# Performance work log

Measured on AMD Instinct MI355X. Metric: run time of the kernel, lower is better.

Reference implementation:

```python
import jax, jax.numpy as jnp
import numpy as np

N_NODES = 100000
N_EDGES = 1600000
F_IN = 8
PERIODS = 18
UNITS = 256     # A3TGCN out_channels (unit_num)
HIDDEN = 256    # MLP hidden_units


def setup_inputs() -> dict:
    key = jax.random.key(0)
    ks = jax.random.split(key, 24)
    g = lambda k, shape, s: (jax.random.normal(k, shape, dtype=jnp.float32) * s)
    inp = {
        "x": g(ks[0], (N_NODES, F_IN, PERIODS), 1.0),
        "edge_index": jax.random.randint(ks[1], (2, N_EDGES), 0, N_NODES, dtype=jnp.int64),
        "edge_weight": jax.random.uniform(ks[2], (N_EDGES,), dtype=jnp.float32),
        # TGCN gate params: GCNConv weight/bias + Linear(2*UNITS, UNITS)
        "Wz": g(ks[3], (F_IN, UNITS), 0.1), "bz": jnp.zeros((UNITS,), jnp.float32),
        "Wlz": g(ks[4], (2 * UNITS, UNITS), 0.05), "blz": jnp.zeros((UNITS,), jnp.float32),
        "Wr": g(ks[5], (F_IN, UNITS), 0.1), "br": jnp.zeros((UNITS,), jnp.float32),
        "Wlr": g(ks[6], (2 * UNITS, UNITS), 0.05), "blr": jnp.zeros((UNITS,), jnp.float32),
        "Wh": g(ks[7], (F_IN, UNITS), 0.1), "bh": jnp.zeros((UNITS,), jnp.float32),
        "Wlh": g(ks[8], (2 * UNITS, UNITS), 0.05), "blh": jnp.zeros((UNITS,), jnp.float32),
        # temporal attention logits
        "att": jax.random.uniform(ks[9], (PERIODS,), dtype=jnp.float32),
        # MLP head
        "W1": g(ks[10], (UNITS, HIDDEN), 0.05), "b1": jnp.zeros((HIDDEN,), jnp.float32),
        "W2": g(ks[11], (HIDDEN, HIDDEN), 0.05), "b2": jnp.zeros((HIDDEN,), jnp.float32),
        "W3": g(ks[12], (HIDDEN, HIDDEN), 0.05), "b3": jnp.zeros((HIDDEN,), jnp.float32),
        "Wo": g(ks[13], (HIDDEN, PERIODS), 0.05), "bo": jnp.zeros((PERIODS,), jnp.float32),
    }
    return inp


def _gcn_norm(edge_index, edge_weight, n_nodes):
    # PyG gcn_norm with add_self_loops=True, improved=False
    src, dst = edge_index[0], edge_index[1]
    loop = jnp.arange(n_nodes, dtype=src.dtype)
    src_a = jnp.concatenate([src, loop])
    dst_a = jnp.concatenate([dst, loop])
    w_a = jnp.concatenate([edge_weight, jnp.ones((n_nodes,), edge_weight.dtype)])
    deg = jax.ops.segment_sum(w_a, dst_a, num_segments=n_nodes)
    dinv = jnp.where(deg > 0, jax.lax.rsqrt(jnp.where(deg > 0, deg, 1.0)), 0.0)
    norm = dinv[src_a] * w_a * dinv[dst_a]
    return src_a, dst_a, norm


def reference(x, edge_index, edge_weight, Wz, bz, Wlz, blz, Wr, br, Wlr, blr,
              Wh, bh, Wlh, blh, att, W1, b1, W2, b2, W3, b3, Wo, bo):
    n_nodes = x.shape[0]
    src, dst, norm = _gcn_norm(edge_index, edge_weight, n_nodes)

    def gconv(X, W, b):
        m = (X @ W)[src] * norm[:, None]                       # [E+N, UNITS]
        return jax.ops.segment_sum(m, dst, num_segments=n_nodes) + b

    probs = jax.nn.softmax(att)

    def step(carry, inp):
        H, acc = carry
        Xt, p = inp                                            # Xt: [N, F_IN]
        Z = jax.nn.sigmoid(jnp.concatenate([gconv(Xt, Wz, bz), H], 1) @ Wlz + blz)
        R = jax.nn.sigmoid(jnp.concatenate([gconv(Xt, Wr, br), H], 1) @ Wlr + blr)
        Ht = jnp.tanh(jnp.concatenate([gconv(Xt, Wh, bh), H * R], 1) @ Wlh + blh)
        H = Z * H + (1.0 - Z) * Ht
        return (H, acc + p * H), None

    xs = jnp.transpose(x, (2, 0, 1))                           # [T, N, F_IN]
    init = (jnp.zeros((n_nodes, UNITS), x.dtype), jnp.zeros((n_nodes, UNITS), x.dtype))
    (_, h), _ = jax.lax.scan(step, init, (xs, probs))

    h = jax.nn.relu(h)
    h = jax.nn.relu(h @ W1 + b1)
    h = jax.nn.relu(h @ W2 + b2)
    h = jax.nn.relu(h @ W3 + b3)
    return h @ Wo + bo                                         # [N, PERIODS]
```

## Files before the change

### kernel.cpp

```cpp
#include <hip/hip_runtime.h>

typedef _Float16 h8 __attribute__((ext_vector_type(8)));
typedef _Float16 h2 __attribute__((ext_vector_type(2)));
typedef float f4 __attribute__((ext_vector_type(4)));

#define N_NODES 100000
#define NPAD    100096
#define N_EDGES 1600000
#define T_P  18
#define U    256
#define KP   288
#define LDW  296
#define NB_SCAN 391

#define LOG2E  1.44269504f
#define LOG2E2 2.88539008f

__global__ void k_init_deg(float* deg){
    int i = blockIdx.x*256 + threadIdx.x;
    if (i < N_NODES) deg[i] = 1.0f;
}
__global__ void k_deg(const int* __restrict__ ei, const float* __restrict__ w, float* deg){
    int e = blockIdx.x*256 + threadIdx.x;
    if (e < N_EDGES) atomicAdd(&deg[ei[N_EDGES + e]], w[e]);
}
__global__ void k_dinv(const float* deg, float* dinv){
    int i = blockIdx.x*256 + threadIdx.x;
    if (i < N_NODES) dinv[i] = rsqrtf(deg[i]);
}
__global__ void k_count(const int* __restrict__ ei, int* cnt){
    int e = blockIdx.x*256 + threadIdx.x;
    if (e < N_EDGES) atomicAdd(&cnt[ei[N_EDGES + e]], 1);
}
__global__ void k_partial(const int* __restrict__ cnt, int* part){
    __shared__ int red[256];
    int b = blockIdx.x, i = b*256 + threadIdx.x;
    red[threadIdx.x] = (i < N_NODES) ? cnt[i] : 0;
    __syncthreads();
    for (int d = 128; d > 0; d >>= 1){
        if (threadIdx.x < d) red[threadIdx.x] += red[threadIdx.x + d];
        __syncthreads();
    }
    if (threadIdx.x == 0) part[b] = red[0];
}
__global__ void k_scan_part(const int* __restrict__ part, int* pbase){
    __shared__ int s[512];
    int tid = threadIdx.x;
    int v = (tid < NB_SCAN) ? part[tid] : 0;
    s[tid] = v; __syncthreads();
    for (int d = 1; d < 512; d <<= 1){
        int t2 = (tid >= d) ? s[tid - d] : 0;
        __syncthreads();
        s[tid] += t2;
        __syncthreads();
    }
    if (tid < NB_SCAN) pbase[tid] = s[tid] - v;
}
__global__ void k_emit(const int* __restrict__ cnt, const int* __restrict__ pbase,
                       int* rowp, int* ccur){
    __shared__ int s[256];
    int b = blockIdx.x, tid = threadIdx.x, i = b*256 + tid;
    int v = (i < N_NODES) ? cnt[i] : 0;
    s[tid] = v; __syncthreads();
    for (int d = 1; d < 256; d <<= 1){
        int t2 = (tid >= d) ? s[tid - d] : 0;
        __syncthreads();
        s[tid] += t2;
        __syncthreads();
    }
    int excl = s[tid] - v + pbase[b];
    if (i < N_NODES){
        rowp[i] = excl; ccur[i] = excl;
        if (i == N_NODES - 1) rowp[N_NODES] = excl + v;
    }
}
__global__ void k_scatter(const int* __restrict__ ei, const float* __restrict__ w,
                          const float* __restrict__ dinv, int* ccur,
                          int* __restrict__ csrc, float* __restrict__ cnrm){
    int e = blockIdx.x*256 + threadIdx.x;
    if (e >= N_EDGES) return;
    int s = ei[e], d = ei[N_EDGES + e];
    int pos = atomicAdd(&ccur[d], 1);
    csrc[pos] = s;
    cnrm[pos] = dinv[s] * w[e] * dinv[d];
}
__global__ void k_gather_nf(const float* __restrict__ x, const float* __restrict__ dinv,
                            const int* __restrict__ rowp, const int* __restrict__ csrc,
                            const float* __restrict__ cnrm, _Float16* __restrict__ AXh){
    int idx = blockIdx.x*256 + threadIdx.x;
    if (idx >= N_NODES*8) return;
    int n = idx >> 3, f = idx & 7;
    float dv = dinv[n];
    float w0 = dv * dv;
    const float* xb = x + (size_t)n*144 + f*18;
    float s[T_P];
    #pragma unroll
    for (int t = 0; t < T_P; t++) s[t] = w0 * xb[t];
    int p1 = rowp[n+1];
    for (int p = rowp[n]; p < p1; p++){
        float w = cnrm[p];
        const float* xs = x + (size_t)csrc[p]*144 + f*18;
        #pragma unroll
        for (int t = 0; t < T_P; t++) s[t] += w * xs[t];
    }
    #pragma unroll
    for (int t = 0; t < T_P; t++)
        AXh[((size_t)t*NPAD + n)*8 + f] = (_Float16)s[t];
}

__global__ void k_probs(const float* att, float* probs){
    if (threadIdx.x == 0 && blockIdx.x == 0){
        float mx = -1e30f;
        for (int t = 0; t < T_P; t++) mx = fmaxf(mx, att[t]);
        float e[T_P], s = 0.f;
        for (int t = 0; t < T_P; t++){ e[t] = __expf(att[t] - mx); s += e[t]; }
        for (int t = 0; t < T_P; t++) probs[t] = e[t] / s;
    }
}
__global__ void k_wprime(const float* Wz, const float* bz, const float* Wlz, const float* blz,
                         const float* Wr, const float* br, const float* Wlr, const float* blr,
                         const float* Wh, const float* bh, const float* Wlh, const float* blh,
                         float* wprime, float* biasg){
    int idx = blockIdx.x*256 + threadIdx.x;
    if (idx >= 3*9*256) return;
    int g = idx / (9*256); int rem = idx - g*9*256;
    int row = rem / 256;   int u = rem - row*256;
    const float* W  = g==0 ? Wz  : (g==1 ? Wr  : Wh);
    const float* Wl = g==0 ? Wlz : (g==1 ? Wlr : Wlh);
    const float* bb = g==0 ? bz  : (g==1 ? br  : bh);
    const float* bl = g==0 ? blz : (g==1 ? blr : blh);
    float s = 0.f;
    if (row < 8){
        for (int c = 0; c < U; c++) s += W[row*U + c] * Wl[c*U + u];
        wprime[(g*8 + row)*U + u] = s;
    } else {
        for (int c = 0; c < U; c++) s += bb[c] * Wl[c*U + u];
        biasg[g*U + u] = s + bl[u];
    }
}
__global__ void k_fill_gates(const float* __restrict__ wprime, const float* __restrict__ Wlz,
                             const float* __restrict__ Wlr, const float* __restrict__ Wlh,
                             _Float16* __restrict__ B1t, _Float16* __restrict__ B2t){
    int idx = blockIdx.x*256 + threadIdx.x;
    if (idx >= 768*KP) return;
    int n = idx / KP, k = idx - n*KP;
    int g = (n < 256) ? 0 : ((n < 512) ? 1 : 2);
    int u = n & 255;
    const float* Wl = g==0 ? Wlz : (g==1 ? Wlr : Wlh);
    float v;
    if (k < 8)        v = wprime[(g*8 + k)*U + u];
    else if (k < 264) v = Wl[(256 + (k - 8))*U + u];
    else              v = 0.f;
    if (n < 512) B1t[(size_t)n*KP + k] = (_Float16)v;
    else         B2t[(size_t)(n - 512)*KP + k] = (_Float16)v;
}
__global__ void k_fill_mlp(const float* __restrict__ W1, const float* __restrict__ W2,
                           const float* __restrict__ W3, const float* __restrict__ Wo,
                           _Float16* W1t, _Float16* W2t, _Float16* W3t, _Float16* WoT){
    int idx = blockIdx.x*256 + threadIdx.x;
    if (idx >= 3*U*KP + 64*KP) return;
    if (idx < 3*U*KP){
        int l = idx / (U*KP); int rem = idx - l*U*KP;
        int n = rem / KP, k = rem - n*KP;
        const float* W = l==0 ? W1 : (l==1 ? W2 : W3);
        _Float16*   Wt = l==0 ? W1t : (l==1 ? W2t : W3t);
        Wt[(size_t)n*KP + k] = (k >= 8 && k < 264) ? (_Float16)W[(size_t)(k-8)*U + n] : (_Float16)0.f;
    } else {
        int rem = idx - 3*U*KP;
        int n = rem / KP, k = rem - n*KP;
        WoT[(size_t)n*KP + k] = (n < T_P && k >= 8 && k < 264) ? (_Float16)Wo[(size_t)(k-8)*T_P + n] : (_Float16)0.f;
    }
}

__device__ __forceinline__ void gemm_pass(const _Float16* sbuf, const _Float16* __restrict__ Bg,
                                          int brow, int lr, int lq, f4* g){
    for (int kt = 0; kt < 9; kt++){
        h8 af[4], bf[2];
        #pragma unroll
        for (int i = 0; i < 4; i++)
            af[i] = *(const h8*)(sbuf + (i*16 + lr)*LDW + kt*32 + lq*8);
        #pragma unroll
        for (int j = 0; j < 2; j++)
            bf[j] = *(const h8*)(Bg + (size_t)(brow + j*16 + lr)*KP + kt*32 + lq*8);
        #pragma unroll
        for (int i = 0; i < 4; i++)
            #pragma unroll
            for (int j = 0; j < 2; j++)
                g[i*2 + j] = __builtin_amdgcn_mfma_f32_16x16x32_f16(af[i], bf[j], g[i*2 + j], 0, 0, 0);
    }
}

__global__ __attribute__((amdgpu_waves_per_eu(2, 2))) __launch_bounds__(512)
void k_fused(const _Float16* __restrict__ AXh,
             const _Float16* __restrict__ B1t, const _Float16* __restrict__ B2t,
             const float* __restrict__ biasg,
             const _Float16* __restrict__ W1t, const _Float16* __restrict__ W2t,
             const _Float16* __restrict__ W3t, const _Float16* __restrict__ WoT,
             const float* __restrict__ b1, const float* __restrict__ b2,
             const float* __restrict__ b3, const float* __restrict__ bo,
             const float* __restrict__ probs, float* __restrict__ dout){
    __shared__ __align__(16) _Float16 sA[64*LDW];
    __shared__ __align__(16) _Float16 sB[64*LDW];
    const int tid  = threadIdx.x;
    const int wave = tid >> 6, lane = tid & 63;
    const int lr = lane & 15, lq = lane >> 4;
    const int wc = wave * 32;
    const int n0 = blockIdx.x * 64;

    {
        uint* w0 = (uint*)sA; uint* w1 = (uint*)sB;
        for (int i = tid; i < 64*LDW/2; i += 512){ w0[i] = 0u; w1[i] = 0u; }
    }
    __syncthreads();
    if (tid < 64)
        *(uint4*)(&sA[tid*LDW]) = *(const uint4*)(AXh + ((size_t)0*NPAD + n0 + tid)*8);
    else if (tid < 128)
        *(uint4*)(&sB[(tid-64)*LDW]) = *(const uint4*)(AXh + ((size_t)0*NPAD + n0 + (tid-64))*8);

    float bz_r[2], br_r[2], bh_r[2];
    #pragma unroll
    for (int j = 0; j < 2; j++){
        int col = wc + j*16 + lr;
        bz_r[j] = -LOG2E  * biasg[col];
        br_r[j] = -LOG2E  * biasg[256 + col];
        bh_r[j] =  LOG2E2 * biasg[512 + col];
    }

    h2 acc[16], hr[16], htr[16];
    h2 z2 = {(_Float16)0.f, (_Float16)0.f};
    #pragma unroll
    for (int k = 0; k < 16; k++){ acc[k] = z2; hr[k] = z2; }

    f4 g[8];
    const f4 fz = {0.f, 0.f, 0.f, 0.f};
    __syncthreads();

    for (int t = 0; t < T_P; t++){
        const float pt = probs[t];
        const int last = (t == T_P - 1);
        uint4 nx;
        if (!last){
            if (tid < 64)
                nx = *(const uint4*)(AXh + ((size_t)(t+1)*NPAD + n0 + tid)*8);
            else if (tid < 128)
                nx = *(const uint4*)(AXh + ((size_t)(t+1)*NPAD + n0 + (tid-64))*8);
        }
        #pragma unroll
        for (int k = 0; k < 8; k++) g[k] = fz;
        gemm_pass(sA, B1t, 256 + wc, lr, lq, g);
        #pragma unroll
        for (int i = 0; i < 4; i++)
            #pragma unroll
            for (int j = 0; j < 2; j++)
                #pragma unroll
                for (int r = 0; r < 4; r++){
                    int v = (i*2 + j)*4 + r;
                    int row = i*16 + lq*4 + r;
                    int col = wc + j*16 + lr;
                    float rr = __builtin_amdgcn_rcpf(
                        1.f + __builtin_amdgcn_exp2f(fmaf(g[i*2 + j][r], -LOG2E, br_r[j])));
                    sB[row*LDW + 8 + col] = (_Float16)((float)hr[v>>1][v&1] * rr);
                }
        __syncthreads();
        #pragma unroll
        for (int k = 0; k < 8; k++) g[k] = fz;
        gemm_pass(sB, B2t, wc, lr, lq, g);
        #pragma unroll
        for (int i = 0; i < 4; i++)
            #pragma unroll
            for (int j = 0; j < 2; j++)
                #pragma unroll
                for (int r = 0; r < 4; r++){
                    int v = (i*2 + j)*4 + r;
                    float e2 = __builtin_amdgcn_exp2f(fmaf(g[i*2 + j][r], LOG2E2, bh_r[j]));
                    htr[v>>1][v&1] = (_Float16)fmaf(-2.f, __builtin_amdgcn_rcpf(e2 + 1.f), 1.f);
                }
        #pragma unroll
        for (int k = 0; k < 8; k++) g[k] = fz;
        gemm_pass(sA, B1t, wc, lr, lq, g);
        __syncthreads();
        #pragma unroll
        for (int i = 0; i < 4; i++)
            #pragma unroll
            for (int j = 0; j < 2; j++)
                #pragma unroll
                for (int r = 0; r < 4; r++){
                    int v = (i*2 + j)*4 + r;
                    int row = i*16 + lq*4 + r;
                    int col = wc + j*16 + lr;
                    float z = __builtin_amdgcn_rcpf(
                        1.f + __builtin_amdgcn_exp2f(fmaf(g[i*2 + j][r], -LOG2E, bz_r[j])));
                    float h  = (float)hr[v>>1][v&1];
                    float ht = (float)htr[v>>1][v&1];
                    float hn = fmaf(z, h - ht, ht);
                    float a  = fmaf(pt, hn, (float)acc[v>>1][v&1]);
                    acc[v>>1][v&1] = (_Float16)a;
                    hr[v>>1][v&1]  = (_Float16)hn;
                    sA[row*LDW + 8 + col] = (_Float16)(last ? fmaxf(a, 0.f) : hn);
                }
        if (!last){
            if (tid < 64)
                *(uint4*)(&sA[tid*LDW]) = nx;
            else if (tid < 128)
                *(uint4*)(&sB[(tid-64)*LDW]) = nx;
        }
        __syncthreads();
    }

    #pragma unroll
    for (int l = 0; l < 3; l++){
        const _Float16* Wt = (l == 0) ? W1t : (l == 1) ? W2t : W3t;
        const float*    bl = (l == 0) ? b1  : (l == 1) ? b2  : b3;
        float blv[2];
        #pragma unroll
        for (int j = 0; j < 2; j++) blv[j] = bl[wc + j*16 + lr];
        #pragma unroll
        for (int k = 0; k < 8; k++) g[k] = fz;
        gemm_pass(sA, Wt, wc, lr, lq, g);
        __syncthreads();
        #pragma unroll
        for (int i = 0; i < 4; i++)
            #pragma unroll
            for (int j = 0; j < 2; j++)
                #pragma unroll
                for (int r = 0; r < 4; r++){
                    int row = i*16 + lq*4 + r;
                    int col = wc + j*16 + lr;
                    sA[row*LDW + 8 + col] = (_Float16)fmaxf(g[i*2 + j][r] + blv[j], 0.f);
                }
        __syncthreads();
    }
    if (wave == 0){
        #pragma unroll
        for (int k = 0; k < 8; k++) g[k] = fz;
        gemm_pass(sA, WoT, 0, lr, lq, g);
        #pragma unroll
        for (int i = 0; i < 4; i++)
            #pragma unroll
            for (int j = 0; j < 2; j++)
                #pragma unroll
                for (int r = 0; r < 4; r++){
                    int row = i*16 + lq*4 + r;
                    int col = j*16 + lr;
                    int gm = n0 + row;
                    if (col < T_P && gm < N_NODES)
                        dout[(size_t)gm*T_P + col] = g[i*2 + j][r] + bo[col];
                }
    }
}

extern "C" void kernel_launch(void* const* d_in, const int* in_sizes, int n_in,
                              void* d_out, int out_size, void* d_ws, size_t ws_size,
                              hipStream_t stream){
    const float* x   = (const float*)d_in[0];
    const int*   ei  = (const int*)  d_in[1];
    const float* ew  = (const float*)d_in[2];
    const float* Wz  = (const float*)d_in[3];  const float* bz  = (const float*)d_in[4];
    const float* Wlz = (const float*)d_in[5];  const float* blz = (const float*)d_in[6];
    const float* Wr  = (const float*)d_in[7];  const float* br  = (const float*)d_in[8];
    const float* Wlr = (const float*)d_in[9];  const float* blr = (const float*)d_in[10];
    const float* Wh  = (const float*)d_in[11]; const float* bh  = (const float*)d_in[12];
    const float* Wlh = (const float*)d_in[13]; const float* blh = (const float*)d_in[14];
    const float* att = (const float*)d_in[15];
    const float* W1  = (const float*)d_in[16]; const float* b1  = (const float*)d_in[17];
    const float* W2  = (const float*)d_in[18]; const float* b2  = (const float*)d_in[19];
    const float* W3  = (const float*)d_in[20]; const float* b3  = (const float*)d_in[21];
    const float* Wo  = (const float*)d_in[22]; const float* bo  = (const float*)d_in[23];
    float* dout = (float*)d_out;

    char* ws = (char*)d_ws; size_t off = 0;
    auto alloc = [&](size_t bytes)->char*{ char* p = ws + off; off += (bytes + 255) & ~(size_t)255; return p; };
    _Float16* AXh   = (_Float16*)alloc((size_t)T_P*NPAD*8*2);
    float*    deg   = (float*)alloc((size_t)N_NODES*4);
    float*    dinv  = (float*)alloc((size_t)N_NODES*4);
    int*      cnt   = (int*)  alloc((size_t)N_NODES*4);
    int*      rowp  = (int*)  alloc(((size_t)N_NODES + 1)*4);
    int*      ccur  = (int*)  alloc((size_t)N_NODES*4);
    int*      csrc  = (int*)  alloc((size_t)N_EDGES*4);
    float*    cnrm  = (float*)alloc((size_t)N_EDGES*4);
    int*      part  = (int*)  alloc((size_t)NB_SCAN*4);
    int*      pbase = (int*)  alloc((size_t)NB_SCAN*4);
    float*    wprime= (float*)alloc((size_t)3*8*U*4);
    float*    biasg = (float*)alloc((size_t)3*U*4);
    _Float16* B1t   = (_Float16*)alloc((size_t)512*KP*2);
    _Float16* B2t   = (_Float16*)alloc((size_t)256*KP*2);
    _Float16* W1t   = (_Float16*)alloc((size_t)U*KP*2);
    _Float16* W2t   = (_Float16*)alloc((size_t)U*KP*2);
    _Float16* W3t   = (_Float16*)alloc((size_t)U*KP*2);
    _Float16* WoT   = (_Float16*)alloc((size_t)64*KP*2);
    float*    probs = (float*)alloc((size_t)T_P*4);

    hipMemsetAsync(AXh, 0, (size_t)T_P*NPAD*8*2, stream);
    hipMemsetAsync(cnt, 0, (size_t)N_NODES*4, stream);

    k_probs<<<1, 64, 0, stream>>>(att, probs);
    k_wprime<<<(3*9*256 + 255)/256, 256, 0, stream>>>(Wz,bz,Wlz,blz, Wr,br,Wlr,blr, Wh,bh,Wlh,blh, wprime, biasg);
    k_fill_gates<<<(768*KP + 255)/256, 256, 0, stream>>>(wprime, Wlz, Wlr, Wlh, B1t, B2t);
    k_fill_mlp<<<(3*U*KP + 64*KP + 255)/256, 256, 0, stream>>>(W1, W2, W3, Wo, W1t, W2t, W3t, WoT);

    k_init_deg<<<(N_NODES + 255)/256, 256, 0, stream>>>(deg);
    k_deg<<<(N_EDGES + 255)/256, 256, 0, stream>>>(ei, ew, deg);
    k_dinv<<<(N_NODES + 255)/256, 256, 0, stream>>>(deg, dinv);
    k_count<<<(N_EDGES + 255)/256, 256, 0, stream>>>(ei, cnt);
    k_partial<<<NB_SCAN, 256, 0, stream>>>(cnt, part);
    k_scan_part<<<1, 512, 0, stream>>>(part, pbase);
    k_emit<<<NB_SCAN, 256, 0, stream>>>(cnt, pbase, rowp, ccur);
    k_scatter<<<(N_EDGES + 255)/256, 256, 0, stream>>>(ei, ew, dinv, ccur, csrc, cnrm);
    k_gather_nf<<<(N_NODES*8 + 255)/256, 256, 0, stream>>>(x, dinv, rowp, csrc, cnrm, AXh);

    k_fused<<<NPAD/64, 512, 0, stream>>>(AXh, B1t, B2t, biasg, W1t, W2t, W3t, WoT,
                                         b1, b2, b3, bo, probs, dout);
}
```

Baseline: 2.200 ms.

## Fuse Z and R gate GEMMs into one pass and drop a barrier per step

The Z and R gate GEMMs share the same A operand in shared memory, so they are now computed in a single pass that reads A fragments once and issues both MFMAs. The H-tilde activation is folded into the final update loop, which removes the htr register array and one __syncthreads per timestep. The next-step X slice for sB is loaded and written within the step instead of being carried over from the previous one. The cost is 16 live f4 accumulators during the fused pass, which raises register pressure under the fixed 2 waves per EU and could cause spills.

```diff
diff --git a/kernel.cpp b/kernel.cpp
--- a/kernel.cpp
+++ b/kernel.cpp
@@ -189,6 +189,27 @@
                 g[i*2 + j] = __builtin_amdgcn_mfma_f32_16x16x32_f16(af[i], bf[j], g[i*2 + j], 0, 0, 0);
     }
 }
+__device__ __forceinline__ void gemm_pass2(const _Float16* sbuf, const _Float16* __restrict__ Bg,
+                                           int browZ, int browR, int lr, int lq, f4* gz, f4* gr){
+    for (int kt = 0; kt < 9; kt++){
+        h8 af[4], bz_[2], br_[2];
+        #pragma unroll
+        for (int i = 0; i < 4; i++)
+            af[i] = *(const h8*)(sbuf + (i*16 + lr)*LDW + kt*32 + lq*8);
+        #pragma unroll
+        for (int j = 0; j < 2; j++){
+            bz_[j] = *(const h8*)(Bg + (size_t)(browZ + j*16 + lr)*KP + kt*32 + lq*8);
+            br_[j] = *(const h8*)(Bg + (size_t)(browR + j*16 + lr)*KP + kt*32 + lq*8);
+        }
+        #pragma unroll
+        for (int i = 0; i < 4; i++)
+            #pragma unroll
+            for (int j = 0; j < 2; j++){
+                gz[i*2 + j] = __builtin_amdgcn_mfma_f32_16x16x32_f16(af[i], bz_[j], gz[i*2 + j], 0, 0, 0);
+                gr[i*2 + j] = __builtin_amdgcn_mfma_f32_16x16x32_f16(af[i], br_[j], gr[i*2 + j], 0, 0, 0);
+            }
+    }
+}
 
 __global__ __attribute__((amdgpu_waves_per_eu(2, 2))) __launch_bounds__(512)
 void k_fused(const _Float16* __restrict__ AXh,
@@ -214,8 +235,6 @@
     __syncthreads();
     if (tid < 64)
         *(uint4*)(&sA[tid*LDW]) = *(const uint4*)(AXh + ((size_t)0*NPAD + n0 + tid)*8);
-    else if (tid < 128)
-        *(uint4*)(&sB[(tid-64)*LDW]) = *(const uint4*)(AXh + ((size_t)0*NPAD + n0 + (tid-64))*8);
 
     float bz_r[2], br_r[2], bh_r[2];
     #pragma unroll
@@ -226,28 +245,27 @@
         bh_r[j] =  LOG2E2 * biasg[512 + col];
     }
 
-    h2 acc[16], hr[16], htr[16];
+    h2 acc[16], hr[16];
     h2 z2 = {(_Float16)0.f, (_Float16)0.f};
     #pragma unroll
     for (int k = 0; k < 16; k++){ acc[k] = z2; hr[k] = z2; }
 
-    f4 g[8];
     const f4 fz = {0.f, 0.f, 0.f, 0.f};
     __syncthreads();
 
     for (int t = 0; t < T_P; t++){
         const float pt = probs[t];
         const int last = (t == T_P - 1);
-        uint4 nx;
-        if (!last){
-            if (tid < 64)
-                nx = *(const uint4*)(AXh + ((size_t)(t+1)*NPAD + n0 + tid)*8);
-            else if (tid < 128)
-                nx = *(const uint4*)(AXh + ((size_t)(t+1)*NPAD + n0 + (tid-64))*8);
+        uint4 ld;
+        if (tid < 64){
+            if (!last) ld = *(const uint4*)(AXh + ((size_t)(t+1)*NPAD + n0 + tid)*8);
+        } else if (tid < 128){
+            ld = *(const uint4*)(AXh + ((size_t)t*NPAD + n0 + (tid-64))*8);
         }
-        #pragma unroll
-        for (int k = 0; k < 8; k++) g[k] = fz;
-        gemm_pass(sA, B1t, 256 + wc, lr, lq, g);
+        f4 gz[8], gr[8];
+        #pragma unroll
+        for (int k = 0; k < 8; k++){ gz[k] = fz; gr[k] = fz; }
+        gemm_pass2(sA, B1t, wc, 256 + wc, lr, lq, gz, gr);
         #pragma unroll
         for (int i = 0; i < 4; i++)
             #pragma unroll
@@ -258,27 +276,16 @@
                     int row = i*16 + lq*4 + r;
                     int col = wc + j*16 + lr;
                     float rr = __builtin_amdgcn_rcpf(
-                        1.f + __builtin_amdgcn_exp2f(fmaf(g[i*2 + j][r], -LOG2E, br_r[j])));
+                        1.f + __builtin_amdgcn_exp2f(fmaf(gr[i*2 + j][r], -LOG2E, br_r[j])));
                     sB[row*LDW + 8 + col] = (_Float16)((float)hr[v>>1][v&1] * rr);
                 }
-        __syncthreads();
+        if (tid >= 64 && tid < 128)
+            *(uint4*)(&sB[(tid-64)*LDW]) = ld;
+        __syncthreads();
+        f4 g[8];
         #pragma unroll
         for (int k = 0; k < 8; k++) g[k] = fz;
         gemm_pass(sB, B2t, wc, lr, lq, g);
-        #pragma unroll
-        for (int i = 0; i < 4; i++)
-            #pragma unroll
-            for (int j = 0; j < 2; j++)
-                #pragma unroll
-                for (int r = 0; r < 4; r++){
-                    int v = (i*2 + j)*4 + r;
-                    float e2 = __builtin_amdgcn_exp2f(fmaf(g[i*2 + j][r], LOG2E2, bh_r[j]));
-                    htr[v>>1][v&1] = (_Float16)fmaf(-2.f, __builtin_amdgcn_rcpf(e2 + 1.f), 1.f);
-                }
-        #pragma unroll
-        for (int k = 0; k < 8; k++) g[k] = fz;
-        gemm_pass(sA, B1t, wc, lr, lq, g);
-        __syncthreads();
         #pragma unroll
         for (int i = 0; i < 4; i++)
             #pragma unroll
@@ -288,22 +295,19 @@
                     int v = (i*2 + j)*4 + r;
                     int row = i*16 + lq*4 + r;
                     int col = wc + j*16 + lr;
-                    float z = __builtin_amdgcn_rcpf(
-                        1.f + __builtin_amdgcn_exp2f(fmaf(g[i*2 + j][r], -LOG2E, bz_r[j])));
+                    float e2 = __builtin_amdgcn_exp2f(fmaf(g[i*2 + j][r], LOG2E2, bh_r[j]));
+                    float ht = fmaf(-2.f, __builtin_amdgcn_rcpf(e2 + 1.f), 1.f);
+                    float z  = __builtin_amdgcn_rcpf(
+                        1.f + __builtin_amdgcn_exp2f(fmaf(gz[i*2 + j][r], -LOG2E, bz_r[j])));
                     float h  = (float)hr[v>>1][v&1];
-                    float ht = (float)htr[v>>1][v&1];
                     float hn = fmaf(z, h - ht, ht);
                     float a  = fmaf(pt, hn, (float)acc[v>>1][v&1]);
                     acc[v>>1][v&1] = (_Float16)a;
                     hr[v>>1][v&1]  = (_Float16)hn;
                     sA[row*LDW + 8 + col] = (_Float16)(last ? fmaxf(a, 0.f) : hn);
                 }
-        if (!last){
-            if (tid < 64)
-                *(uint4*)(&sA[tid*LDW]) = nx;
-            else if (tid < 128)
-                *(uint4*)(&sB[(tid-64)*LDW]) = nx;
-        }
+        if (!last && tid < 64)
+            *(uint4*)(&sA[tid*LDW]) = ld;
         __syncthreads();
     }
 
@@ -314,6 +318,7 @@
         float blv[2];
         #pragma unroll
         for (int j = 0; j < 2; j++) blv[j] = bl[wc + j*16 + lr];
+        f4 g[8];
         #pragma unroll
         for (int k = 0; k < 8; k++) g[k] = fz;
         gemm_pass(sA, Wt, wc, lr, lq, g);
@@ -331,6 +336,7 @@
         __syncthreads();
     }
     if (wave == 0){
+        f4 g[8];
         #pragma unroll
         for (int k = 0; k < 8; k++) g[k] = fz;
         gemm_pass(sA, WoT, 0, lr, lq, g);
```

New measurement: 2.420 ms. 10.0% more time.
